# Kernel optimization log

Measured on AMD Instinct MI355X. Metric: run time of the kernel, lower is better.

## Reference

```python
import jax, jax.numpy as jnp
import numpy as np


def setup_inputs() -> dict:
    key = jax.random.key(0)
    k1, k2 = jax.random.split(key)
    B, S, H = 64, 512, 1024
    sequence_output = jax.random.normal(k1, (B, S, H), dtype=jnp.float32)
    valid_ids = jax.random.randint(k2, (B, S), 0, 2, dtype=jnp.int32)
    return {"sequence_output": sequence_output, "valid_ids": valid_ids}


def reference(sequence_output, valid_ids):
    # Per batch row: move positions where valid_ids==1 to the front (stable
    # order), zero-pad the remainder -- vectorized stream compaction.
    B, S, H = sequence_output.shape
    mask = (valid_ids == 1)                                  # [B, S] bool
    # stable argsort on (1 - mask): valid positions first, original order kept
    order = jnp.argsort(jnp.where(mask, 0, 1), axis=-1, stable=True)  # [B, S]
    gathered = jnp.take_along_axis(sequence_output, order[:, :, None], axis=1)
    n_valid = jnp.sum(mask, axis=-1, keepdims=True)          # [B, 1]
    keep = jnp.arange(S)[None, :] < n_valid                  # [B, S]
    return gathered * keep[:, :, None].astype(sequence_output.dtype)
```

## Files before the change

kernel.cpp:

```cpp
#include <hip/hip_runtime.h>
#include <hip/hip_bf16.h>


__global__ void build_index_kernel(const int* __restrict__ valid,
                                   int* __restrict__ src,
                                   int* __restrict__ nvalid,
                                   int S) {
    const int b = blockIdx.x;
    const int s = threadIdx.x;
    const int lane = threadIdx.x & 63;
    const int wave = threadIdx.x >> 6;

    const int v = (valid[b * S + s] == 1) ? 1 : 0;

    unsigned long long bal = __ballot(v != 0);
    unsigned long long lower = (lane == 0) ? 0ull : (bal & ((1ull << lane) - 1ull));
    int in_wave_prefix = __popcll(lower);
    int wave_total = __popcll(bal);

    __shared__ int wsum[8];
    __shared__ int woff[8];
    if (lane == 0) wsum[wave] = wave_total;
    __syncthreads();
    if (threadIdx.x == 0) {
        int acc = 0;
        #pragma unroll
        for (int w = 0; w < 8; ++w) { woff[w] = acc; acc += wsum[w]; }
        nvalid[b] = acc;
    }
    __syncthreads();

    if (v) {
        src[b * S + woff[wave] + in_wave_prefix] = s;
    }
}

__global__ void gather_rows_kernel(const float4* __restrict__ in,
                                   float4* __restrict__ out,
                                   const int* __restrict__ src,
                                   const int* __restrict__ nvalid,
                                   int S, int H4) {
    const int bid = blockIdx.x;
    const int b = bid >> 9;
    const int j = bid & 511;
    const int t = threadIdx.x;

    const long long orow = (long long)bid * H4;
    if (j < nvalid[b]) {
        const int s = src[b * S + j];
        const long long irow = ((long long)b * S + s) * (long long)H4;
        out[orow + t] = in[irow + t];
    } else {
        out[orow + t] = make_float4(0.f, 0.f, 0.f, 0.f);
    }
}

extern "C" void kernel_launch(void* const* d_in, const int* in_sizes, int n_in,
                              void* d_out, int out_size, void* d_ws, size_t ws_size,
                              hipStream_t stream) {
    const float* seq = (const float*)d_in[0];
    const int* valid = (const int*)d_in[1];

    const int S = 512;
    const int BS = in_sizes[1];
    const int B = BS / S;
    const int H = in_sizes[0] / BS;
    const int H4 = H / 4;

    int* src = (int*)d_ws;
    int* nvalid = src + BS;

    build_index_kernel<<<B, S, 0, stream>>>(valid, src, nvalid, S);

    gather_rows_kernel<<<BS, H4, 0, stream>>>(
        (const float4*)seq, (float4*)d_out, src, nvalid, S, H4);
}
```

Measured before the change: 36.64 us.

## Fuse index building into gather kernel with per-block ballot rank select

Drops the separate index-building kernel. Each gather block now reads its batch row's 512 valid flags, ballots them into eight 64-bit words in shared memory, and finds the j-th set bit through popcount prefix sums plus bit clearing. This removes one launch and the workspace round trip, at the cost of every block redundantly reading 2KB of flags and doing a serial bit-select loop. It also switches to nontemporal loads and stores, and hardcodes H=1024 and S=512.

After: 46.84 us. +27.8%, slower.

```diff
diff --git a/kernel.cpp b/kernel.cpp
--- a/kernel.cpp
+++ b/kernel.cpp
@@ -2,57 +2,57 @@
 #include <hip/hip_bf16.h>
 
 
-__global__ void build_index_kernel(const int* __restrict__ valid,
-                                   int* __restrict__ src,
-                                   int* __restrict__ nvalid,
-                                   int S) {
-    const int b = blockIdx.x;
-    const int s = threadIdx.x;
-    const int lane = threadIdx.x & 63;
-    const int wave = threadIdx.x >> 6;
+typedef float v4f __attribute__((ext_vector_type(4)));
 
-    const int v = (valid[b * S + s] == 1) ? 1 : 0;
-
-    unsigned long long bal = __ballot(v != 0);
-    unsigned long long lower = (lane == 0) ? 0ull : (bal & ((1ull << lane) - 1ull));
-    int in_wave_prefix = __popcll(lower);
-    int wave_total = __popcll(bal);
-
-    __shared__ int wsum[8];
-    __shared__ int woff[8];
-    if (lane == 0) wsum[wave] = wave_total;
-    __syncthreads();
-    if (threadIdx.x == 0) {
-        int acc = 0;
-        #pragma unroll
-        for (int w = 0; w < 8; ++w) { woff[w] = acc; acc += wsum[w]; }
-        nvalid[b] = acc;
-    }
-    __syncthreads();
-
-    if (v) {
-        src[b * S + woff[wave] + in_wave_prefix] = s;
-    }
-}
-
-__global__ void gather_rows_kernel(const float4* __restrict__ in,
-                                   float4* __restrict__ out,
-                                   const int* __restrict__ src,
-                                   const int* __restrict__ nvalid,
-                                   int S, int H4) {
+__global__ __launch_bounds__(256) void compact_fused_kernel(
+    const v4f* __restrict__ in,
+    const int* __restrict__ valid,
+    v4f* __restrict__ out) {
     const int bid = blockIdx.x;
     const int b = bid >> 9;
     const int j = bid & 511;
     const int t = threadIdx.x;
+    const int lane = t & 63;
+    const int wave = t >> 6;
 
-    const long long orow = (long long)bid * H4;
-    if (j < nvalid[b]) {
-        const int s = src[b * S + j];
-        const long long irow = ((long long)b * S + s) * (long long)H4;
-        out[orow + t] = in[irow + t];
-    } else {
-        out[orow + t] = make_float4(0.f, 0.f, 0.f, 0.f);
+    const int base = b << 9;
+    const int v0 = (valid[base + t] == 1);
+    const int v1 = (valid[base + t + 256] == 1);
+    unsigned long long bal0 = __ballot(v0 != 0);
+    unsigned long long bal1 = __ballot(v1 != 0);
+
+    __shared__ unsigned long long words[8];
+    if (lane == 0) {
+        words[wave] = bal0;
+        words[wave + 4] = bal1;
     }
+    __syncthreads();
+
+    int cnt[8];
+    int nvalid = 0;
+    #pragma unroll
+    for (int w = 0; w < 8; ++w) { cnt[w] = __popcll(words[w]); nvalid += cnt[w]; }
+
+    const long long orow = (long long)bid << 8;
+
+    if (j >= nvalid) {
+        v4f z = {0.f, 0.f, 0.f, 0.f};
+        __builtin_nontemporal_store(z, &out[orow + t]);
+        return;
+    }
+
+    int w = 0, rem = j;
+    #pragma unroll
+    for (int i = 0; i < 7; ++i) {
+        if (rem >= cnt[w]) { rem -= cnt[w]; ++w; }
+    }
+    unsigned long long x = words[w];
+    for (int i = 0; i < rem; ++i) x &= (x - 1);
+    const int s = (w << 6) + (int)__builtin_ctzll(x);
+
+    const long long irow = ((long long)(base + s)) << 8;
+    const v4f val = __builtin_nontemporal_load(&in[irow + t]);
+    __builtin_nontemporal_store(val, &out[orow + t]);
 }
 
 extern "C" void kernel_launch(void* const* d_in, const int* in_sizes, int n_in,
@@ -61,17 +61,8 @@
     const float* seq = (const float*)d_in[0];
     const int* valid = (const int*)d_in[1];
 
-    const int S = 512;
     const int BS = in_sizes[1];
-    const int B = BS / S;
-    const int H = in_sizes[0] / BS;
-    const int H4 = H / 4;
 
-    int* src = (int*)d_ws;
-    int* nvalid = src + BS;
-
-    build_index_kernel<<<B, S, 0, stream>>>(valid, src, nvalid, S);
-
-    gather_rows_kernel<<<BS, H4, 0, stream>>>(
-        (const float4*)seq, (float4*)d_out, src, nvalid, S, H4);
+    compact_fused_kernel<<<BS, 256, 0, stream>>>(
+        (const v4f*)seq, valid, (v4f*)d_out);
 }
```
